# Performance work log

Measured on AMD Instinct MI355X. Metric: run time of the kernel, lower is better.

## Reference

```python
import math
import jax, jax.numpy as jnp
import numpy as np

D_MODEL = 1024
N_HEADS = 16
D_K = D_MODEL // N_HEADS
THETA = 10000.0
B, S = 2, 2048


def setup_inputs() -> dict:
    key = jax.random.key(0)
    k1, k2, k3 = jax.random.split(key, 3)
    x = jax.random.normal(k1, (B, S, D_MODEL), dtype=jnp.float32)
    token_positions = jnp.arange(B * S, dtype=jnp.int32).reshape(B, S)
    std_qkv = math.sqrt(2.0 / (D_MODEL + 3 * D_MODEL))
    std_o = math.sqrt(2.0 / (D_MODEL + D_MODEL))
    W_qkv = jax.random.truncated_normal(k2, -3.0, 3.0, (3 * D_MODEL, D_MODEL), dtype=jnp.float32) * std_qkv
    W_o = jax.random.truncated_normal(k3, -3.0, 3.0, (D_MODEL, D_MODEL), dtype=jnp.float32) * std_o
    return {"x": x, "W_qkv": W_qkv, "W_o": W_o, "token_positions": token_positions}


def _rope(x, pos):
    # x: (B, H, S, D_K); pos: (B, S) int
    half = D_K // 2
    inv_freq = 1.0 / (THETA ** (jnp.arange(0, D_K, 2, dtype=jnp.float32) / D_K))  # (half,)
    # pos_extended = pos[:, None, :] -> freqs (B, 1, S, half)
    freqs = pos[:, None, :, None].astype(jnp.float32) * inv_freq
    cos, sin = jnp.cos(freqs), jnp.sin(freqs)
    xr = x.reshape(*x.shape[:-1], half, 2)
    x1, x2 = xr[..., 0], xr[..., 1]
    out = jnp.stack([x1 * cos - x2 * sin, x2 * cos + x1 * sin], axis=-1)
    return out.reshape(x.shape)


def reference(x, W_qkv, W_o, token_positions):
    seq_len = x.shape[-2]
    qkv = jnp.einsum('bsi,oi->bso', x, W_qkv)
    q, k, v = jnp.split(qkv, 3, axis=-1)
    # (B, S, H*D) -> (B, H, S, D)
    def to_heads(t):
        return t.reshape(t.shape[0], t.shape[1], N_HEADS, D_K).transpose(0, 2, 1, 3)
    q, k, v = to_heads(q), to_heads(k), to_heads(v)
    q = _rope(q, token_positions)
    k = _rope(k, token_positions)
    scores = jnp.einsum('bhnd,bhmd->bhnm', q, k) / math.sqrt(D_K)
    causal = jnp.tril(jnp.ones((seq_len, seq_len), dtype=bool))
    scores = jnp.where(causal, scores, -jnp.inf)
    attn = jax.nn.softmax(scores, axis=-1)
    out = jnp.einsum('bhnm,bhmd->bhnd', attn, v)
    out = out.transpose(0, 2, 1, 3).reshape(x.shape[0], seq_len, D_MODEL)
    return jnp.einsum('bsi,oi->bso', out, W_o)
```

## Files before the change

kernel.cpp:

```cpp
#include <hip/hip_runtime.h>
#include <cmath>
#include <type_traits>

typedef __bf16 bf16;
typedef bf16 bf16x4 __attribute__((ext_vector_type(4)));
typedef bf16 bf16x8 __attribute__((ext_vector_type(8)));
typedef float f32x4 __attribute__((ext_vector_type(4)));

#define MFMA16(a, b, c) __builtin_amdgcn_mfma_f32_16x16x32_bf16(a, b, c, 0, 0, 0)

__global__ __launch_bounds__(256) void cvt_all(
    const float* __restrict__ x, const float* __restrict__ wqkv,
    const float* __restrict__ wo, bf16* __restrict__ xb,
    bf16* __restrict__ wqkvb, bf16* __restrict__ wob) {
  int i = (blockIdx.x * 256 + threadIdx.x) * 4;
  const float* src;
  bf16* dst;
  if (i < (4 << 20)) {
    src = x + i; dst = xb + i;
  } else if (i < (7 << 20)) {
    src = wqkv + (i - (4 << 20)); dst = wqkvb + (i - (4 << 20));
  } else {
    src = wo + (i - (7 << 20)); dst = wob + (i - (7 << 20));
  }
  const f32x4 v = *(const f32x4*)src;
  bf16x4 o = {(bf16)v[0], (bf16)v[1], (bf16)v[2], (bf16)v[3]};
  *(bf16x4*)dst = o;
}

template <int EPI>
__global__ __launch_bounds__(256) void gemm_nt(
    const bf16* __restrict__ A, const bf16* __restrict__ Bm,
    const int* __restrict__ tokpos,
    bf16* __restrict__ out0, bf16* __restrict__ out1, bf16* __restrict__ out2,
    float* __restrict__ outF, int N) {
  __shared__ __align__(16) bf16 As[2][128 * 32];
  __shared__ __align__(16) bf16 Bs[2][128 * 32];
  const int tid = threadIdx.x;
  const int w = tid >> 6, lane = tid & 63, quad = lane >> 4, m16 = lane & 15;
  const int m0 = blockIdx.y * 128, n0 = blockIdx.x * 128;
  const int wm = (w >> 1) * 64, wn = (w & 1) * 64;

  f32x4 acc[4][4] = {};

  const int row0 = tid >> 2, ch = tid & 3;
  const bf16* Ag0 = A + (size_t)(m0 + row0) * 1024 + ch * 8;
  const bf16* Ag1 = A + (size_t)(m0 + 64 + row0) * 1024 + ch * 8;
  const bf16* Bg0 = Bm + (size_t)(n0 + row0) * 1024 + ch * 8;
  const bf16* Bg1 = Bm + (size_t)(n0 + 64 + row0) * 1024 + ch * 8;

  bf16x8 ra0, ra1, rb0, rb1;
  auto LOAD = [&](int k0) {
    ra0 = *(const bf16x8*)(Ag0 + k0);
    ra1 = *(const bf16x8*)(Ag1 + k0);
    rb0 = *(const bf16x8*)(Bg0 + k0);
    rb1 = *(const bf16x8*)(Bg1 + k0);
  };
  auto WRITE = [&](int p) {
    *(bf16x8*)(As[p] + tid * 8) = ra0;
    *(bf16x8*)(As[p] + 2048 + tid * 8) = ra1;
    *(bf16x8*)(Bs[p] + tid * 8) = rb0;
    *(bf16x8*)(Bs[p] + 2048 + tid * 8) = rb1;
  };

  LOAD(0);
  WRITE(0);
  __syncthreads();

  int p = 0;
  for (int k0 = 0; k0 < 1024; k0 += 32) {
    const bool more = (k0 + 32) < 1024;
    if (more) LOAD(k0 + 32);
    bf16x8 af[4], bfr[4];
#pragma unroll
    for (int mi = 0; mi < 4; ++mi)
      af[mi] = *(const bf16x8*)(As[p] + (wm + mi * 16 + m16) * 32 + quad * 8);
#pragma unroll
    for (int ni = 0; ni < 4; ++ni)
      bfr[ni] = *(const bf16x8*)(Bs[p] + (wn + ni * 16 + m16) * 32 + quad * 8);
#pragma unroll
    for (int mi = 0; mi < 4; ++mi)
#pragma unroll
      for (int ni = 0; ni < 4; ++ni)
        acc[mi][ni] = MFMA16(af[mi], bfr[ni], acc[mi][ni]);
    if (more) {
      WRITE(1 - p);
      __syncthreads();
      p ^= 1;
    }
  }

  if constexpr (EPI == 0) {
#pragma unroll
    for (int mi = 0; mi < 4; ++mi) {
      int rowb = m0 + wm + mi * 16 + quad * 4;
#pragma unroll
      for (int r = 0; r < 4; ++r) {
        size_t off = (size_t)(rowb + r) * N + n0 + wn;
#pragma unroll
        for (int ni = 0; ni < 4; ++ni)
          outF[off + ni * 16 + m16] = acc[mi][ni][r];
      }
    }
  } else {
#pragma unroll
    for (int mi = 0; mi < 4; ++mi) {
      int rowb = m0 + wm + mi * 16 + quad * 4;
      int pos4[4];
#pragma unroll
      for (int r = 0; r < 4; ++r) pos4[r] = tokpos[rowb + r];
#pragma unroll
      for (int ni = 0; ni < 4; ++ni) {
        int col = n0 + wn + ni * 16 + m16;
        int sec = col >> 10, f = col & 1023, h = f >> 6, d = f & 63;
        if (sec == 2) {
#pragma unroll
          for (int r = 0; r < 4; ++r) {
            int row = rowb + r;
            int bb = row >> 11, s = row & 2047;
            out2[((size_t)(bb * 16 + h) * 64 + d) * 2048 + s] =
                (bf16)acc[mi][ni][r];
          }
        } else {
          float inv = __expf(-(float)(d & ~1) * (9.2103403719762f / 64.f));
          bf16* dst = sec ? out1 : out0;
          const float sc = sec ? 1.0f : 0.125f;
#pragma unroll
          for (int r = 0; r < 4; ++r) {
            float v = acc[mi][ni][r];
            float vp = __shfl_xor(v, 1);
            float ang = (float)pos4[r] * inv;
            float cs, sn;
            __sincosf(ang, &sn, &cs);
            float ov = (d & 1) ? (v * cs + vp * sn) : (v * cs - vp * sn);
            ov *= sc;
            int row = rowb + r;
            int bb = row >> 11, s = row & 2047;
            dst[((size_t)(bb * 16 + h) * 2048 + s) * 64 + d] = (bf16)ov;
          }
        }
      }
    }
  }
}

__global__ __launch_bounds__(256) void attn_kernel(
    const bf16* __restrict__ Q, const bf16* __restrict__ K,
    const bf16* __restrict__ Vt, bf16* __restrict__ O) {
  __shared__ __align__(16) bf16 KP[2][64 * 72];
  __shared__ __align__(16) bf16 VP[2][64 * 72];
  __shared__ __align__(16) bf16 PS[2][4][16 * 72];
  const int tid = threadIdx.x;
  const int w = tid >> 6, lane = tid & 63, quad = lane >> 4, m16 = lane & 15;
  const int bh = blockIdx.x;
  const int j = blockIdx.y;
  const int qtA = j, qtB = 31 - j;
  const int q0A = qtA * 64, q0B = qtB * 64;
  const bf16* Qb = Q + (size_t)bh * 2048 * 64;
  const bf16* Kb = K + (size_t)bh * 2048 * 64;
  const bf16* Vb = Vt + (size_t)bh * 64 * 2048;

  const int ch0 = w * 8, ch1 = (w + 4) * 8;
  const bf16* Kg = Kb + (size_t)lane * 64;
  const bf16* Vg = Vb + (size_t)lane * 2048;

  const bf16* qrowA = Qb + (size_t)(q0A + w * 16 + m16) * 64;
  const bf16* qrowB = Qb + (size_t)(q0B + w * 16 + m16) * 64;
  bf16x8 aqA[2], aqB[2];
  aqA[0] = *(const bf16x8*)(qrowA + quad * 8);
  aqA[1] = *(const bf16x8*)(qrowA + 32 + quad * 8);
  aqB[0] = *(const bf16x8*)(qrowB + quad * 8);
  aqB[1] = *(const bf16x8*)(qrowB + 32 + quad * 8);

  bf16x8 rk0, rk1, rv0, rv1;
  auto PREFETCH = [&](int kt) {
    rk0 = *(const bf16x8*)(Kg + (size_t)kt * 64 * 64 + ch0);
    rk1 = *(const bf16x8*)(Kg + (size_t)kt * 64 * 64 + ch1);
    rv0 = *(const bf16x8*)(Vg + kt * 64 + ch0);
    rv1 = *(const bf16x8*)(Vg + kt * 64 + ch1);
  };
  auto STAGE = [&](int p) {
    *(bf16x8*)(KP[p] + lane * 72 + ch0) = rk0;
    *(bf16x8*)(KP[p] + lane * 72 + ch1) = rk1;
    *(bf16x8*)(VP[p] + lane * 72 + ch0) = rv0;
    *(bf16x8*)(VP[p] + lane * 72 + ch1) = rv1;
  };

  PREFETCH(0);
  STAGE(0);
  __syncthreads();

  f32x4 oA[4] = {}, oB[4] = {};
  float lA[4] = {0.f, 0.f, 0.f, 0.f}, lB[4] = {0.f, 0.f, 0.f, 0.f};
  const int qrel = w * 16 + quad * 4;

  auto strip = [&](int p, const bf16x8* aq, f32x4* o, float* lp, bf16* ps,
                   auto diag_c) {
    constexpr bool DIAG = decltype(diag_c)::value;
    f32x4 sa[4] = {};
#pragma unroll
    for (int kk = 0; kk < 2; ++kk)
#pragma unroll
      for (int ni = 0; ni < 4; ++ni) {
        bf16x8 bk = *(const bf16x8*)(KP[p] + (ni * 16 + m16) * 72 + kk * 32 +
                                     quad * 8);
        sa[ni] = MFMA16(aq[kk], bk, sa[ni]);
      }
#pragma unroll
    for (int r = 0; r < 4; ++r) {
#pragma unroll
      for (int ni = 0; ni < 4; ++ni) {
        float pp = exp2f(fmaf(sa[ni][r], 1.44269504f, -11.5415603f));
        if constexpr (DIAG)
          if ((ni * 16 + m16) > qrel + r) pp = 0.f;
        lp[r] += pp;
        ps[(quad * 4 + r) * 72 + ni * 16 + m16] = (bf16)pp;
      }
    }
    bf16x8 ap[2];
    ap[0] = *(const bf16x8*)(ps + m16 * 72 + quad * 8);
    ap[1] = *(const bf16x8*)(ps + m16 * 72 + 32 + quad * 8);
#pragma unroll
    for (int kk = 0; kk < 2; ++kk)
#pragma unroll
      for (int ng = 0; ng < 4; ++ng) {
        bf16x8 bv = *(const bf16x8*)(VP[p] + (ng * 16 + m16) * 72 + kk * 32 +
                                     quad * 8);
        o[ng] = MFMA16(ap[kk], bv, o[ng]);
      }
  };
  constexpr std::false_type ND{};
  constexpr std::true_type DG{};

  int p = 0;
  for (int kt = 0; kt <= qtB; ++kt) {
    const bool more = kt < qtB;
    if (more) PREFETCH(kt + 1);
    if (kt < qtA) {
      strip(p, aqB, oB, lB, PS[1][w], ND);
      strip(p, aqA, oA, lA, PS[0][w], ND);
    } else if (kt == qtA) {
      strip(p, aqB, oB, lB, PS[1][w], ND);
      strip(p, aqA, oA, lA, PS[0][w], DG);
    } else if (more) {
      strip(p, aqB, oB, lB, PS[1][w], ND);
    } else {
      strip(p, aqB, oB, lB, PS[1][w], DG);
    }
    if (more) {
      STAGE(1 - p);
      __syncthreads();
      p ^= 1;
    }
  }

  const int b = bh >> 4, h = bh & 15;
  auto epilogue = [&](f32x4* o, float* lp, int q0) {
#pragma unroll
    for (int r = 0; r < 4; ++r) {
      float l = lp[r];
      l += __shfl_xor(l, 1);
      l += __shfl_xor(l, 2);
      l += __shfl_xor(l, 4);
      l += __shfl_xor(l, 8);
      float inv_l = 1.f / l;
      int s = q0 + w * 16 + quad * 4 + r;
      size_t rowoff = (size_t)(b * 2048 + s) * 1024 + h * 64;
#pragma unroll
      for (int ng = 0; ng < 4; ++ng)
        O[rowoff + ng * 16 + m16] = (bf16)(o[ng][r] * inv_l);
    }
  };
  epilogue(oA, lA, q0A);
  epilogue(oB, lB, q0B);
}

extern "C" void kernel_launch(void* const* d_in, const int* in_sizes, int n_in,
                              void* d_out, int out_size, void* d_ws, size_t ws_size,
                              hipStream_t stream) {
  (void)in_sizes; (void)n_in; (void)out_size; (void)ws_size;
  const float* x = (const float*)d_in[0];
  const float* Wqkv = (const float*)d_in[1];
  const float* Wo = (const float*)d_in[2];
  const int* tokpos = (const int*)d_in[3];
  float* out = (float*)d_out;

  const size_t NEL = (size_t)2 * 16 * 2048 * 64;
  bf16* Qws = (bf16*)d_ws;
  bf16* Kws = Qws + NEL;
  bf16* Vtw = Kws + NEL;
  bf16* Ows = Vtw + NEL;
  bf16* xb  = Ows + NEL;
  bf16* Wqkvb = xb + NEL;
  bf16* Wob = Wqkvb + (size_t)3072 * 1024;

  cvt_all<<<8192, 256, 0, stream>>>(x, Wqkv, Wo, xb, Wqkvb, Wob);

  gemm_nt<1><<<dim3(24, 32), 256, 0, stream>>>(xb, Wqkvb, tokpos, Qws, Kws,
                                               Vtw, nullptr, 3072);
  attn_kernel<<<dim3(32, 16), 256, 0, stream>>>(Qws, Kws, Vtw, Ows);
  gemm_nt<0><<<dim3(8, 32), 256, 0, stream>>>(Ows, Wob, nullptr, nullptr,
                                              nullptr, nullptr, out, 1024);
}
```

Before: 202.9 us.

## Software-pipeline attention loop: compute next tile's QK^T while doing softmax/PV

Switches K/V shared staging to a triple buffer and restructures the main loop so the QK^T MFMAs for tile kt+1 are issued before the exp/PV work of tile kt, with global prefetch two tiles ahead. The aim is to overlap MFMA latency with softmax ALU work and hide global load latency. The P scratch buffer is shared between the A and B strips, and the diagonal mask becomes a runtime flag instead of a compile-time specialization. This raises LDS use and register pressure, since two sets of score accumulators stay live.

```diff
diff --git a/kernel.cpp b/kernel.cpp
--- a/kernel.cpp
+++ b/kernel.cpp
@@ -1,6 +1,5 @@
 #include <hip/hip_runtime.h>
 #include <cmath>
-#include <type_traits>
 
 typedef __bf16 bf16;
 typedef bf16 bf16x4 __attribute__((ext_vector_type(4)));
@@ -147,9 +146,9 @@
 __global__ __launch_bounds__(256) void attn_kernel(
     const bf16* __restrict__ Q, const bf16* __restrict__ K,
     const bf16* __restrict__ Vt, bf16* __restrict__ O) {
-  __shared__ __align__(16) bf16 KP[2][64 * 72];
-  __shared__ __align__(16) bf16 VP[2][64 * 72];
-  __shared__ __align__(16) bf16 PS[2][4][16 * 72];
+  __shared__ __align__(16) bf16 KP[3][64 * 72];
+  __shared__ __align__(16) bf16 VP[3][64 * 72];
+  __shared__ __align__(16) bf16 PS[4][16 * 72];
   const int tid = threadIdx.x;
   const int w = tid >> 6, lane = tid & 63, quad = lane >> 4, m16 = lane & 15;
   const int bh = blockIdx.x;
@@ -188,16 +187,11 @@
 
   PREFETCH(0);
   STAGE(0);
+  PREFETCH(1);
+  STAGE(1);
   __syncthreads();
 
-  f32x4 oA[4] = {}, oB[4] = {};
-  float lA[4] = {0.f, 0.f, 0.f, 0.f}, lB[4] = {0.f, 0.f, 0.f, 0.f};
-  const int qrel = w * 16 + quad * 4;
-
-  auto strip = [&](int p, const bf16x8* aq, f32x4* o, float* lp, bf16* ps,
-                   auto diag_c) {
-    constexpr bool DIAG = decltype(diag_c)::value;
-    f32x4 sa[4] = {};
+  auto QK = [&](int p, const bf16x8* aq, f32x4* sa) {
 #pragma unroll
     for (int kk = 0; kk < 2; ++kk)
 #pragma unroll
@@ -206,13 +200,20 @@
                                      quad * 8);
         sa[ni] = MFMA16(aq[kk], bk, sa[ni]);
       }
+  };
+
+  f32x4 oA[4] = {}, oB[4] = {};
+  float lA[4] = {0.f, 0.f, 0.f, 0.f}, lB[4] = {0.f, 0.f, 0.f, 0.f};
+  const int qrel = w * 16 + quad * 4;
+
+  auto SOFTPV = [&](int p, const f32x4* sa, f32x4* o, float* lp, bool diag) {
+    bf16* ps = PS[w];
 #pragma unroll
     for (int r = 0; r < 4; ++r) {
 #pragma unroll
       for (int ni = 0; ni < 4; ++ni) {
         float pp = exp2f(fmaf(sa[ni][r], 1.44269504f, -11.5415603f));
-        if constexpr (DIAG)
-          if ((ni * 16 + m16) > qrel + r) pp = 0.f;
+        if (diag && (ni * 16 + m16) > qrel + r) pp = 0.f;
         lp[r] += pp;
         ps[(quad * 4 + r) * 72 + ni * 16 + m16] = (bf16)pp;
       }
@@ -229,29 +230,30 @@
         o[ng] = MFMA16(ap[kk], bv, o[ng]);
       }
   };
-  constexpr std::false_type ND{};
-  constexpr std::true_type DG{};
-
-  int p = 0;
+
+  f32x4 saA[4] = {}, saB[4] = {};
+  QK(0, aqB, saB);
+  QK(0, aqA, saA);
+
+  int pc = 0, pn = 1, pst = 2;
   for (int kt = 0; kt <= qtB; ++kt) {
     const bool more = kt < qtB;
-    if (more) PREFETCH(kt + 1);
-    if (kt < qtA) {
-      strip(p, aqB, oB, lB, PS[1][w], ND);
-      strip(p, aqA, oA, lA, PS[0][w], ND);
-    } else if (kt == qtA) {
-      strip(p, aqB, oB, lB, PS[1][w], ND);
-      strip(p, aqA, oA, lA, PS[0][w], DG);
-    } else if (more) {
-      strip(p, aqB, oB, lB, PS[1][w], ND);
-    } else {
-      strip(p, aqB, oB, lB, PS[1][w], DG);
-    }
-    if (more) {
-      STAGE(1 - p);
-      __syncthreads();
-      p ^= 1;
-    }
+    const bool stage2 = (kt + 2) <= qtB;
+    if (stage2) PREFETCH(kt + 2);
+
+    f32x4 saBn[4] = {}, saAn[4] = {};
+    if (more) QK(pn, aqB, saBn);
+    if (kt + 1 <= qtA) QK(pn, aqA, saAn);
+
+    SOFTPV(pc, saB, oB, lB, kt == qtB);
+    if (kt <= qtA) SOFTPV(pc, saA, oA, lA, kt == qtA);
+
+    if (stage2) STAGE(pst);
+    if (more) __syncthreads();
+
+#pragma unroll
+    for (int i = 0; i < 4; ++i) { saB[i] = saBn[i]; saA[i] = saAn[i]; }
+    int t = pc; pc = pn; pn = pst; pst = t;
   }
 
   const int b = bh >> 4, h = bh & 15;
```

New measurement: 198.5 us. 1.02x faster.
